# Optimization experiments

Hardware: AMD Instinct MI355X
Metric: run time of the kernel (lower is better)

Reference implementation:

```python
import jax, jax.numpy as jnp
import numpy as np


def conv2d_same(x, w, b):
    # x: (B,C,H,W), w: (O,I,3,3) -> 3x3 'same' conv, stride 1
    y = jax.lax.conv_general_dilated(
        x, w, window_strides=(1, 1), padding=((1, 1), (1, 1)),
        dimension_numbers=("NCHW", "OIHW", "NCHW"))
    return y + b[None, :, None, None]


def setup_inputs() -> dict:
    key = jax.random.key(0)
    ks = jax.random.split(key, 7)
    B, F, E, H, W = 16, 64, 16, 64, 64
    fan2d = F * 9
    state = jax.random.normal(ks[0], (B, F, H, W), dtype=jnp.float32)
    pre_w = jax.random.normal(ks[1], (F, F, 3, 3), dtype=jnp.float32) / np.sqrt(fan2d)
    pre_b = jax.random.normal(ks[2], (F,), dtype=jnp.float32) * 0.01
    attn_w = jax.random.normal(ks[3], (E, F, 3, 3), dtype=jnp.float32) / np.sqrt(fan2d)
    attn_b = jax.random.normal(ks[4], (E,), dtype=jnp.float32) * 0.01
    c3_w = jax.random.normal(ks[5], (F, F), dtype=jnp.float32) / np.sqrt(F)
    c3_b = jax.random.normal(ks[6], (F,), dtype=jnp.float32) * 0.01
    return {"state": state, "pre_w": pre_w, "pre_b": pre_b,
            "attn_w": attn_w, "attn_b": attn_b, "c3_w": c3_w, "c3_b": c3_b}


def reference(state, pre_w, pre_b, attn_w, attn_b, c3_w, c3_b):
    # pre_conv + relu
    x = jax.nn.relu(conv2d_same(state, pre_w, pre_b))
    # visattn_conv + sigmoid -> (B,E,H,W)
    attn = jax.nn.sigmoid(conv2d_same(x, attn_w, attn_b))
    # einsum 'bfyx,beyx->bfeyx'
    x5 = state[:, :, None, :, :] * attn[:, None, :, :, :]  # (B,F,E,H,W)
    # Conv3d kernel (1,1,1) with padding (0,1,1): zero-pad H,W by 1,
    # then pointwise linear over F. Output spatial dims become (E, H+2, W+2).
    x5 = jnp.pad(x5, ((0, 0), (0, 0), (0, 0), (1, 1), (1, 1)))
    y = jnp.einsum("of,bfeyx->boeyx", c3_w, x5) + c3_b[None, :, None, None, None]
    y = jax.nn.relu(y)
    # permute (0,2,1,3,4) then mean over last two dims -> (B,E,F)
    out = jnp.mean(y, axis=(-1, -2)).transpose(0, 2, 1)
    return out, attn
```

## Files before the change

### kernel.cpp

```cpp
#include <hip/hip_runtime.h>
#include <math.h>

constexpr int B = 16, F = 64, E = 16, H = 64, W = 64;
constexpr int XP = 66;
constexpr int CP = 72;
constexpr int YSTRIDE = XP * F;

typedef __bf16 bf16x8 __attribute__((ext_vector_type(8)));
typedef __bf16 bf16x4 __attribute__((ext_vector_type(4)));
typedef float f32x16 __attribute__((ext_vector_type(16)));
typedef float f32x4 __attribute__((ext_vector_type(4)));

__global__ __launch_bounds__(256) void prep_kernel(
    const float* __restrict__ state, const float* __restrict__ pre_w,
    const float* __restrict__ attn_w, const float* __restrict__ c3_w,
    __bf16* __restrict__ xTs, __bf16* __restrict__ wA1,
    __bf16* __restrict__ wA2, __bf16* __restrict__ wT3b,
    float* __restrict__ out0)
{
    __shared__ float s_t[64][68];
    const int blk = blockIdx.x;
    const int tid = threadIdx.x;

    if (blk < 1024) {
        const int b = blk >> 6, y = blk & 63;
        {
            int c = tid >> 2, x0 = (tid & 3) * 16;
            const float* src = state + ((size_t)(b * F + c) * H + y) * W + x0;
            #pragma unroll
            for (int q = 0; q < 4; ++q)
                *(float4*)&s_t[c][x0 + 4 * q] = *(const float4*)(src + 4 * q);
        }
        __syncthreads();
        __bf16* dst = xTs + (size_t)(b * H + y) * YSTRIDE;
        #pragma unroll
        for (int i = 0; i < 2; ++i) {
            int t = tid + i * 256;
            int x = t >> 3, cg = t & 7;
            bf16x8 v;
            #pragma unroll
            for (int j = 0; j < 8; ++j) v[j] = (__bf16)s_t[cg * 8 + j][x];
            *(bf16x8*)(dst + (x + 1) * F + cg * 8) = v;
        }
        if (tid < 16) {
            int bd = tid >> 3, cg = tid & 7;
            bf16x8 z = {};
            *(bf16x8*)(dst + (bd ? 65 : 0) * F + cg * 8) = z;
        }
    } else if (blk < 1168) {
        int idx = (blk - 1024) * 256 + tid;
        if (idx < 64 * 576) {
            int o = idx / 576, rem = idx - o * 576, t = rem >> 6, c = rem & 63;
            wA1[idx] = (__bf16)pre_w[(o * 64 + c) * 9 + t];
        }
        if (idx < 16 * 576) {
            int e = idx / 576, rem = idx - e * 576, t = rem >> 6, c = rem & 63;
            wA2[idx] = (__bf16)attn_w[(e * 64 + c) * 9 + t];
        }
        if (idx < 64 * 64) {
            wT3b[idx] = (__bf16)c3_w[idx];
        }
    } else {
        int idx = (blk - 1168) * 256 + tid;
        float4 z = {0.f, 0.f, 0.f, 0.f};
        *(float4*)(out0 + idx * 4) = z;
    }
}

__global__ __launch_bounds__(256) void mega_kernel(
    const __bf16* __restrict__ xTs, const __bf16* __restrict__ wA1,
    const __bf16* __restrict__ wA2, const __bf16* __restrict__ wT3b,
    const float* __restrict__ pre_b, const float* __restrict__ attn_b,
    const float* __restrict__ c3_b,
    float* __restrict__ attn_out, float* __restrict__ out)
{
    __shared__ __align__(16) char smem[63616];
    const int b = blockIdx.y, yp = blockIdx.x;
    const int tid = threadIdx.x;
    const int wave = tid >> 6, lane = tid & 63;
    const int y0 = yp * 2;

    __bf16* s_in = (__bf16*)smem;
    __bf16* sxo  = (__bf16*)smem;
    float (*s_attn)[64][16] = (float(*)[64][16])(smem + 38016);
    float (*s_sp)[68] = (float(*)[68])(smem + 46208);

    for (int t = tid; t < 6 * XP * 8; t += 256) {
        int r = t / (XP * 8), rem = t - r * (XP * 8);
        int x = rem >> 3, cg = rem & 7;
        int yy = y0 - 2 + r;
        bf16x8 v = {};
        if (yy >= 0 && yy < H)
            v = *(const bf16x8*)(xTs + (size_t)(b * H + yy) * YSTRIDE + x * F + cg * 8);
        *(bf16x8*)(s_in + (r * XP + x) * CP + cg * 8) = v;
    }
    __syncthreads();

    {
        const int n = lane & 31, kh = lane >> 5;
        const int yr = y0 - 1 + wave;
        f32x16 acc[4] = {};
        const bool valid = (yr >= 0 && yr < H);
        if (valid) {
            #pragma unroll
            for (int dy = 0; dy < 3; ++dy) {
                #pragma unroll
                for (int dx = 0; dx < 3; ++dx) {
                    const int t9 = dy * 3 + dx;
                    const __bf16* bB = s_in + ((wave + dy) * XP + (n + dx)) * CP + kh * 8;
                    #pragma unroll
                    for (int cq = 0; cq < 4; ++cq) {
                        const int ko = cq * 16 + kh * 8;
                        bf16x8 a0 = *(const bf16x8*)(wA1 + n * 576 + t9 * 64 + ko);
                        bf16x8 a1 = *(const bf16x8*)(wA1 + (32 + n) * 576 + t9 * 64 + ko);
                        bf16x8 b0 = *(const bf16x8*)(bB + cq * 16);
                        bf16x8 b1 = *(const bf16x8*)(bB + 32 * CP + cq * 16);
                        acc[0] = __builtin_amdgcn_mfma_f32_32x32x16_bf16(a0, b0, acc[0], 0, 0, 0);
                        acc[1] = __builtin_amdgcn_mfma_f32_32x32x16_bf16(a0, b1, acc[1], 0, 0, 0);
                        acc[2] = __builtin_amdgcn_mfma_f32_32x32x16_bf16(a1, b0, acc[2], 0, 0, 0);
                        acc[3] = __builtin_amdgcn_mfma_f32_32x32x16_bf16(a1, b1, acc[3], 0, 0, 0);
                    }
                }
            }
        }
        __syncthreads();

        __bf16* orow = sxo + wave * XP * CP;
        #pragma unroll
        for (int mt = 0; mt < 2; ++mt)
            #pragma unroll
            for (int g = 0; g < 4; ++g) {
                int o0 = mt * 32 + kh * 4 + g * 8;
                f32x4 b4 = *(const f32x4*)(pre_b + o0);
                bf16x4 v0 = {}, v1 = {};
                if (valid) {
                    #pragma unroll
                    for (int r = 0; r < 4; ++r) {
                        v0[r] = (__bf16)fmaxf(acc[mt * 2 + 0][g * 4 + r] + b4[r], 0.f);
                        v1[r] = (__bf16)fmaxf(acc[mt * 2 + 1][g * 4 + r] + b4[r], 0.f);
                    }
                }
                *(bf16x4*)(orow + (n + 1) * CP + o0) = v0;
                *(bf16x4*)(orow + (n + 33) * CP + o0) = v1;
            }
        if (tid < 64) {
            int r = tid >> 4, bd = (tid >> 3) & 1, cg = tid & 7;
            bf16x8 z = {};
            *(bf16x8*)(sxo + (r * XP + (bd ? 65 : 0)) * CP + cg * 8) = z;
        }
    }
    __syncthreads();

    const int rw = wave >> 1, nt2 = wave & 1;
    const int n16 = lane & 15, quad = lane >> 4;
    f32x4 acc2[2] = {};
    {
        const __bf16* aB = wA2 + n16 * 576 + quad * 8;
        #pragma unroll
        for (int dy = 0; dy < 3; ++dy)
            #pragma unroll
            for (int dx = 0; dx < 3; ++dx) {
                const int t9 = dy * 3 + dx;
                #pragma unroll
                for (int cq = 0; cq < 2; ++cq) {
                    bf16x8 a = *(const bf16x8*)(aB + t9 * 64 + cq * 32);
                    #pragma unroll
                    for (int i = 0; i < 2; ++i) {
                        const __bf16* bp = sxo +
                            ((rw + dy) * XP + (nt2 * 32 + i * 16 + n16 + dx)) * CP
                            + quad * 8 + cq * 32;
                        acc2[i] = __builtin_amdgcn_mfma_f32_16x16x32_bf16(
                            a, *(const bf16x8*)bp, acc2[i], 0, 0, 0);
                    }
                }
            }
    }

    #pragma unroll
    for (int i = 0; i < 2; ++i) {
        int x = nt2 * 32 + i * 16 + n16;
        #pragma unroll
        for (int r = 0; r < 4; ++r) {
            int e = quad * 4 + r;
            float val = acc2[i][r] + attn_b[e];
            float sg = 1.f / (1.f + __expf(-val));
            attn_out[((size_t)(b * E + e) * H + (y0 + rw)) * W + x] = sg;
            s_attn[rw][x][e] = sg;
        }
    }
    __syncthreads();

    const int combo = tid & 63;
    const int eg = combo >> 4, og = combo & 15, psub = tid >> 6;
    f32x4 cb4 = ((const f32x4*)c3_b)[og];
    float vsum[4] = {0.f, 0.f, 0.f, 0.f};

    for (int rr = 0; rr < 2; ++rr) {
        {
            const int mt = wave & 1, nt = wave >> 1;
            const int n = lane & 31, kh = lane >> 5;
            const __bf16* bBase = xTs + (size_t)(b * H + y0 + rr) * YSTRIDE
                                  + (nt * 32 + n + 1) * F + kh * 8;
            const __bf16* aBase = wT3b + (mt * 32 + n) * 64 + kh * 8;
            f32x16 acc = {};
            #pragma unroll
            for (int cq = 0; cq < 4; ++cq) {
                bf16x8 a  = *(const bf16x8*)(aBase + cq * 16);
                bf16x8 bb = *(const bf16x8*)(bBase + cq * 16);
                acc = __builtin_amdgcn_mfma_f32_32x32x16_bf16(a, bb, acc, 0, 0, 0);
            }
            #pragma unroll
            for (int g = 0; g < 4; ++g)
                #pragma unroll
                for (int r = 0; r < 4; ++r)
                    s_sp[nt * 32 + n][mt * 32 + kh * 4 + g * 8 + r] = acc[g * 4 + r];
        }
        __syncthreads();

        float accl[4][4] = {};
        #pragma unroll 2
        for (int pp = 0; pp < 16; ++pp) {
            int p = psub * 16 + pp;
            f32x4 a4 = *(const f32x4*)&s_attn[rr][p][eg * 4];
            f32x4 s4 = *(const f32x4*)&s_sp[p][og * 4];
            #pragma unroll
            for (int i = 0; i < 4; ++i)
                #pragma unroll
                for (int j = 0; j < 4; ++j)
                    accl[i][j] += fmaxf(fmaf(a4[i], s4[j], cb4[j]), 0.f);
        }
        __syncthreads();
        float* s_part = &s_sp[0][0];
        #pragma unroll
        for (int i = 0; i < 4; ++i)
            #pragma unroll
            for (int j = 0; j < 4; ++j)
                s_part[(psub * 64 + combo) * 16 + i * 4 + j] = accl[i][j];
        __syncthreads();
        {
            int cmb = tid >> 2, ii = tid & 3;
            #pragma unroll
            for (int j = 0; j < 4; ++j) {
                float v = 0.f;
                #pragma unroll
                for (int ps = 0; ps < 4; ++ps)
                    v += s_part[(ps * 64 + cmb) * 16 + ii * 4 + j];
                vsum[j] += v;
            }
        }
        __syncthreads();
    }
    {
        int cmb = tid >> 2, ii = tid & 3;
        int e = (cmb >> 4) * 4 + ii;
        #pragma unroll
        for (int j = 0; j < 4; ++j) {
            int o = (cmb & 15) * 4 + j;
            float add = vsum[j] * (1.f / 4356.f);
            if (yp == 0) add += 260.f * fmaxf(c3_b[o], 0.f) * (1.f / 4356.f);
            atomicAdd(&out[(b * E + e) * F + o], add);
        }
    }
}

extern "C" void kernel_launch(void* const* d_in, const int* in_sizes, int n_in,
                              void* d_out, int out_size, void* d_ws, size_t ws_size,
                              hipStream_t stream) {
    (void)in_sizes; (void)n_in; (void)out_size; (void)ws_size;
    const float* state  = (const float*)d_in[0];
    const float* pre_w  = (const float*)d_in[1];
    const float* pre_b  = (const float*)d_in[2];
    const float* attn_w = (const float*)d_in[3];
    const float* attn_b = (const float*)d_in[4];
    const float* c3_w   = (const float*)d_in[5];
    const float* c3_b   = (const float*)d_in[6];

    float* out      = (float*)d_out;
    float* attn_out = out + B * E * F;

    char* ws = (char*)d_ws;
    constexpr size_t XT_BYTES = (size_t)B * H * YSTRIDE * 2;
    __bf16* xTs  = (__bf16*)ws;
    __bf16* wA1  = (__bf16*)(ws + XT_BYTES);
    __bf16* wA2  = (__bf16*)(ws + XT_BYTES + 73728);
    __bf16* wT3b = (__bf16*)(ws + XT_BYTES + 73728 + 18432);

    prep_kernel<<<1184, 256, 0, stream>>>(state, pre_w, attn_w, c3_w,
                                          xTs, wA1, wA2, wT3b, out);
    mega_kernel<<<dim3(H / 2, B), 256, 0, stream>>>(xTs, wA1, wA2, wT3b,
                                                    pre_b, attn_b, c3_b,
                                                    attn_out, out);
}
```

Measured before the change: 116.1 us.

## Double mega_kernel block size to 512 threads and split work across 8 waves

```diff
diff --git a/kernel.cpp b/kernel.cpp
--- a/kernel.cpp
+++ b/kernel.cpp
@@ -67,7 +67,7 @@
     }
 }
 
-__global__ __launch_bounds__(256) void mega_kernel(
+__global__ __launch_bounds__(512, 4) void mega_kernel(
     const __bf16* __restrict__ xTs, const __bf16* __restrict__ wA1,
     const __bf16* __restrict__ wA2, const __bf16* __restrict__ wT3b,
     const float* __restrict__ pre_b, const float* __restrict__ attn_b,
@@ -84,8 +84,9 @@
     __bf16* sxo  = (__bf16*)smem;
     float (*s_attn)[64][16] = (float(*)[64][16])(smem + 38016);
     float (*s_sp)[68] = (float(*)[68])(smem + 46208);
-
-    for (int t = tid; t < 6 * XP * 8; t += 256) {
+    float* s_part = (float*)smem;
+
+    for (int t = tid; t < 6 * XP * 8; t += 512) {
         int r = t / (XP * 8), rem = t - r * (XP * 8);
         int x = rem >> 3, cg = rem & 7;
         int yy = y0 - 2 + r;
@@ -97,52 +98,49 @@
     __syncthreads();
 
     {
+        const int r1 = wave >> 1, nt = wave & 1;
         const int n = lane & 31, kh = lane >> 5;
-        const int yr = y0 - 1 + wave;
-        f32x16 acc[4] = {};
+        const int yr = y0 - 1 + r1;
         const bool valid = (yr >= 0 && yr < H);
+        f32x16 acc0 = {}, acc1 = {};
         if (valid) {
             #pragma unroll
             for (int dy = 0; dy < 3; ++dy) {
                 #pragma unroll
                 for (int dx = 0; dx < 3; ++dx) {
                     const int t9 = dy * 3 + dx;
-                    const __bf16* bB = s_in + ((wave + dy) * XP + (n + dx)) * CP + kh * 8;
+                    const __bf16* bB = s_in + ((r1 + dy) * XP + (nt * 32 + n + dx)) * CP + kh * 8;
                     #pragma unroll
                     for (int cq = 0; cq < 4; ++cq) {
                         const int ko = cq * 16 + kh * 8;
                         bf16x8 a0 = *(const bf16x8*)(wA1 + n * 576 + t9 * 64 + ko);
                         bf16x8 a1 = *(const bf16x8*)(wA1 + (32 + n) * 576 + t9 * 64 + ko);
-                        bf16x8 b0 = *(const bf16x8*)(bB + cq * 16);
-                        bf16x8 b1 = *(const bf16x8*)(bB + 32 * CP + cq * 16);
-                        acc[0] = __builtin_amdgcn_mfma_f32_32x32x16_bf16(a0, b0, acc[0], 0, 0, 0);
-                        acc[1] = __builtin_amdgcn_mfma_f32_32x32x16_bf16(a0, b1, acc[1], 0, 0, 0);
-                        acc[2] = __builtin_amdgcn_mfma_f32_32x32x16_bf16(a1, b0, acc[2], 0, 0, 0);
-                        acc[3] = __builtin_amdgcn_mfma_f32_32x32x16_bf16(a1, b1, acc[3], 0, 0, 0);
+                        bf16x8 bb = *(const bf16x8*)(bB + cq * 16);
+                        acc0 = __builtin_amdgcn_mfma_f32_32x32x16_bf16(a0, bb, acc0, 0, 0, 0);
+                        acc1 = __builtin_amdgcn_mfma_f32_32x32x16_bf16(a1, bb, acc1, 0, 0, 0);
                     }
                 }
             }
         }
         __syncthreads();
 
-        __bf16* orow = sxo + wave * XP * CP;
-        #pragma unroll
-        for (int mt = 0; mt < 2; ++mt)
-            #pragma unroll
-            for (int g = 0; g < 4; ++g) {
-                int o0 = mt * 32 + kh * 4 + g * 8;
-                f32x4 b4 = *(const f32x4*)(pre_b + o0);
-                bf16x4 v0 = {}, v1 = {};
-                if (valid) {
-                    #pragma unroll
-                    for (int r = 0; r < 4; ++r) {
-                        v0[r] = (__bf16)fmaxf(acc[mt * 2 + 0][g * 4 + r] + b4[r], 0.f);
-                        v1[r] = (__bf16)fmaxf(acc[mt * 2 + 1][g * 4 + r] + b4[r], 0.f);
-                    }
+        __bf16* orow = sxo + r1 * XP * CP;
+        #pragma unroll
+        for (int g = 0; g < 4; ++g) {
+            int o0 = kh * 4 + g * 8;
+            f32x4 b40 = *(const f32x4*)(pre_b + o0);
+            f32x4 b41 = *(const f32x4*)(pre_b + 32 + o0);
+            bf16x4 v0 = {}, v1 = {};
+            if (valid) {
+                #pragma unroll
+                for (int r = 0; r < 4; ++r) {
+                    v0[r] = (__bf16)fmaxf(acc0[g * 4 + r] + b40[r], 0.f);
+                    v1[r] = (__bf16)fmaxf(acc1[g * 4 + r] + b41[r], 0.f);
                 }
-                *(bf16x4*)(orow + (n + 1) * CP + o0) = v0;
-                *(bf16x4*)(orow + (n + 33) * CP + o0) = v1;
-            }
+            }
+            *(bf16x4*)(orow + (nt * 32 + n + 1) * CP + o0) = v0;
+            *(bf16x4*)(orow + (nt * 32 + n + 1) * CP + 32 + o0) = v1;
+        }
         if (tid < 64) {
             int r = tid >> 4, bd = (tid >> 3) & 1, cg = tid & 7;
             bf16x8 z = {};
@@ -151,10 +149,10 @@
     }
     __syncthreads();
 
-    const int rw = wave >> 1, nt2 = wave & 1;
-    const int n16 = lane & 15, quad = lane >> 4;
-    f32x4 acc2[2] = {};
     {
+        const int rw = wave >> 2, xq = wave & 3;
+        const int n16 = lane & 15, quad = lane >> 4;
+        f32x4 acc2 = {};
         const __bf16* aB = wA2 + n16 * 576 + quad * 8;
         #pragma unroll
         for (int dy = 0; dy < 3; ++dy)
@@ -164,25 +162,17 @@
                 #pragma unroll
                 for (int cq = 0; cq < 2; ++cq) {
                     bf16x8 a = *(const bf16x8*)(aB + t9 * 64 + cq * 32);
-                    #pragma unroll
-                    for (int i = 0; i < 2; ++i) {
-                        const __bf16* bp = sxo +
-                            ((rw + dy) * XP + (nt2 * 32 + i * 16 + n16 + dx)) * CP
-                            + quad * 8 + cq * 32;
-                        acc2[i] = __builtin_amdgcn_mfma_f32_16x16x32_bf16(
-                            a, *(const bf16x8*)bp, acc2[i], 0, 0, 0);
-                    }
+                    const __bf16* bp = sxo +
+                        ((rw + dy) * XP + (xq * 16 + n16 + dx)) * CP + quad * 8 + cq * 32;
+                    acc2 = __builtin_amdgcn_mfma_f32_16x16x32_bf16(
+                        a, *(const bf16x8*)bp, acc2, 0, 0, 0);
                 }
             }
-    }
-
-    #pragma unroll
-    for (int i = 0; i < 2; ++i) {
-        int x = nt2 * 32 + i * 16 + n16;
+        const int x = xq * 16 + n16;
         #pragma unroll
         for (int r = 0; r < 4; ++r) {
             int e = quad * 4 + r;
-            float val = acc2[i][r] + attn_b[e];
+            float val = acc2[r] + attn_b[e];
             float sg = 1.f / (1.f + __expf(-val));
             attn_out[((size_t)(b * E + e) * H + (y0 + rw)) * W + x] = sg;
             s_attn[rw][x][e] = sg;
@@ -196,7 +186,7 @@
     float vsum[4] = {0.f, 0.f, 0.f, 0.f};
 
     for (int rr = 0; rr < 2; ++rr) {
-        {
+        if (wave < 4) {
             const int mt = wave & 1, nt = wave >> 1;
             const int n = lane & 31, kh = lane >> 5;
             const __bf16* bBase = xTs + (size_t)(b * H + y0 + rr) * YSTRIDE
@@ -218,9 +208,9 @@
         __syncthreads();
 
         float accl[4][4] = {};
-        #pragma unroll 2
-        for (int pp = 0; pp < 16; ++pp) {
-            int p = psub * 16 + pp;
+        #pragma unroll
+        for (int pp = 0; pp < 8; ++pp) {
+            int p = psub * 8 + pp;
             f32x4 a4 = *(const f32x4*)&s_attn[rr][p][eg * 4];
             f32x4 s4 = *(const f32x4*)&s_sp[p][og * 4];
             #pragma unroll
@@ -230,27 +220,26 @@
                     accl[i][j] += fmaxf(fmaf(a4[i], s4[j], cb4[j]), 0.f);
         }
         __syncthreads();
-        float* s_part = &s_sp[0][0];
         #pragma unroll
         for (int i = 0; i < 4; ++i)
             #pragma unroll
             for (int j = 0; j < 4; ++j)
                 s_part[(psub * 64 + combo) * 16 + i * 4 + j] = accl[i][j];
         __syncthreads();
-        {
+        if (tid < 256) {
             int cmb = tid >> 2, ii = tid & 3;
             #pragma unroll
             for (int j = 0; j < 4; ++j) {
                 float v = 0.f;
                 #pragma unroll
-                for (int ps = 0; ps < 4; ++ps)
+                for (int ps = 0; ps < 8; ++ps)
                     v += s_part[(ps * 64 + cmb) * 16 + ii * 4 + j];
                 vsum[j] += v;
             }
         }
         __syncthreads();
     }
-    {
+    if (tid < 256) {
         int cmb = tid >> 2, ii = tid & 3;
         int e = (cmb >> 4) * 4 + ii;
         #pragma unroll
@@ -287,7 +276,7 @@
 
     prep_kernel<<<1184, 256, 0, stream>>>(state, pre_w, attn_w, c3_w,
                                           xTs, wA1, wA2, wT3b, out);
-    mega_kernel<<<dim3(H / 2, B), 256, 0, stream>>>(xTs, wA1, wA2, wT3b,
+    mega_kernel<<<dim3(H / 2, B), 512, 0, stream>>>(xTs, wA1, wA2, wT3b,
                                                     pre_b, attn_b, c3_b,
                                                     attn_out, out);
 }
```

New measurement: 149.4 us. 28.7% more time.

## Split conv1 input staging into channel halves to shrink LDS and drop syncs

Applied to the files above, without the earlier changes.

```diff
diff --git a/kernel.cpp b/kernel.cpp
--- a/kernel.cpp
+++ b/kernel.cpp
@@ -4,6 +4,7 @@
 constexpr int B = 16, F = 64, E = 16, H = 64, W = 64;
 constexpr int XP = 66;
 constexpr int CP = 72;
+constexpr int CPH = 40;
 constexpr int YSTRIDE = XP * F;
 
 typedef __bf16 bf16x8 __attribute__((ext_vector_type(8)));
@@ -67,14 +68,14 @@
     }
 }
 
-__global__ __launch_bounds__(256) void mega_kernel(
+__global__ __launch_bounds__(256, 3) void mega_kernel(
     const __bf16* __restrict__ xTs, const __bf16* __restrict__ wA1,
     const __bf16* __restrict__ wA2, const __bf16* __restrict__ wT3b,
     const float* __restrict__ pre_b, const float* __restrict__ attn_b,
     const float* __restrict__ c3_b,
     float* __restrict__ attn_out, float* __restrict__ out)
 {
-    __shared__ __align__(16) char smem[63616];
+    __shared__ __align__(16) char smem[46208];
     const int b = blockIdx.y, yp = blockIdx.x;
     const int tid = threadIdx.x;
     const int wave = tid >> 6, lane = tid & 63;
@@ -83,38 +84,42 @@
     __bf16* s_in = (__bf16*)smem;
     __bf16* sxo  = (__bf16*)smem;
     float (*s_attn)[64][16] = (float(*)[64][16])(smem + 38016);
-    float (*s_sp)[68] = (float(*)[68])(smem + 46208);
-
-    for (int t = tid; t < 6 * XP * 8; t += 256) {
-        int r = t / (XP * 8), rem = t - r * (XP * 8);
-        int x = rem >> 3, cg = rem & 7;
-        int yy = y0 - 2 + r;
-        bf16x8 v = {};
-        if (yy >= 0 && yy < H)
-            v = *(const bf16x8*)(xTs + (size_t)(b * H + yy) * YSTRIDE + x * F + cg * 8);
-        *(bf16x8*)(s_in + (r * XP + x) * CP + cg * 8) = v;
-    }
-    __syncthreads();
-
-    {
-        const int n = lane & 31, kh = lane >> 5;
-        const int yr = y0 - 1 + wave;
-        f32x16 acc[4] = {};
-        const bool valid = (yr >= 0 && yr < H);
+    float (*s_sp)[68] = (float(*)[68])smem;
+    float* s_part = (float*)(smem + 17408);
+
+    const int n = lane & 31, kh = lane >> 5;
+    const int yr = y0 - 1 + wave;
+    const bool valid = (yr >= 0 && yr < H);
+    f32x16 acc[4] = {};
+
+    #pragma unroll
+    for (int h = 0; h < 2; ++h) {
+        if (h) __syncthreads();
+        for (int t = tid; t < 6 * XP * 4; t += 256) {
+            int r = t / (XP * 4), rem = t - r * (XP * 4);
+            int x = rem >> 2, cg = rem & 3;
+            int yy = y0 - 2 + r;
+            bf16x8 v = {};
+            if (yy >= 0 && yy < H)
+                v = *(const bf16x8*)(xTs + (size_t)(b * H + yy) * YSTRIDE
+                                     + x * F + h * 32 + cg * 8);
+            *(bf16x8*)(s_in + (r * XP + x) * CPH + cg * 8) = v;
+        }
+        __syncthreads();
         if (valid) {
             #pragma unroll
             for (int dy = 0; dy < 3; ++dy) {
                 #pragma unroll
                 for (int dx = 0; dx < 3; ++dx) {
                     const int t9 = dy * 3 + dx;
-                    const __bf16* bB = s_in + ((wave + dy) * XP + (n + dx)) * CP + kh * 8;
+                    const __bf16* bB = s_in + ((wave + dy) * XP + (n + dx)) * CPH + kh * 8;
                     #pragma unroll
-                    for (int cq = 0; cq < 4; ++cq) {
-                        const int ko = cq * 16 + kh * 8;
-                        bf16x8 a0 = *(const bf16x8*)(wA1 + n * 576 + t9 * 64 + ko);
-                        bf16x8 a1 = *(const bf16x8*)(wA1 + (32 + n) * 576 + t9 * 64 + ko);
+                    for (int cq = 0; cq < 2; ++cq) {
+                        const int ko_w = h * 32 + cq * 16 + kh * 8;
+                        bf16x8 a0 = *(const bf16x8*)(wA1 + n * 576 + t9 * 64 + ko_w);
+                        bf16x8 a1 = *(const bf16x8*)(wA1 + (32 + n) * 576 + t9 * 64 + ko_w);
                         bf16x8 b0 = *(const bf16x8*)(bB + cq * 16);
-                        bf16x8 b1 = *(const bf16x8*)(bB + 32 * CP + cq * 16);
+                        bf16x8 b1 = *(const bf16x8*)(bB + 32 * CPH + cq * 16);
                         acc[0] = __builtin_amdgcn_mfma_f32_32x32x16_bf16(a0, b0, acc[0], 0, 0, 0);
                         acc[1] = __builtin_amdgcn_mfma_f32_32x32x16_bf16(a0, b1, acc[1], 0, 0, 0);
                         acc[2] = __builtin_amdgcn_mfma_f32_32x32x16_bf16(a1, b0, acc[2], 0, 0, 0);
@@ -123,8 +128,10 @@
                 }
             }
         }
-        __syncthreads();
-
+    }
+    __syncthreads();
+
+    {
         __bf16* orow = sxo + wave * XP * CP;
         #pragma unroll
         for (int mt = 0; mt < 2; ++mt)
@@ -198,10 +205,10 @@
     for (int rr = 0; rr < 2; ++rr) {
         {
             const int mt = wave & 1, nt = wave >> 1;
-            const int n = lane & 31, kh = lane >> 5;
+            const int ns = lane & 31, khs = lane >> 5;
             const __bf16* bBase = xTs + (size_t)(b * H + y0 + rr) * YSTRIDE
-                                  + (nt * 32 + n + 1) * F + kh * 8;
-            const __bf16* aBase = wT3b + (mt * 32 + n) * 64 + kh * 8;
+                                  + (nt * 32 + ns + 1) * F + khs * 8;
+            const __bf16* aBase = wT3b + (mt * 32 + ns) * 64 + khs * 8;
             f32x16 acc = {};
             #pragma unroll
             for (int cq = 0; cq < 4; ++cq) {
@@ -213,7 +220,7 @@
             for (int g = 0; g < 4; ++g)
                 #pragma unroll
                 for (int r = 0; r < 4; ++r)
-                    s_sp[nt * 32 + n][mt * 32 + kh * 4 + g * 8 + r] = acc[g * 4 + r];
+                    s_sp[nt * 32 + ns][mt * 32 + khs * 4 + g * 8 + r] = acc[g * 4 + r];
         }
         __syncthreads();
 
@@ -229,8 +236,6 @@
                 for (int j = 0; j < 4; ++j)
                     accl[i][j] += fmaxf(fmaf(a4[i], s4[j], cb4[j]), 0.f);
         }
-        __syncthreads();
-        float* s_part = &s_sp[0][0];
         #pragma unroll
         for (int i = 0; i < 4; ++i)
             #pragma unroll
@@ -248,7 +253,6 @@
                 vsum[j] += v;
             }
         }
-        __syncthreads();
     }
     {
         int cmb = tid >> 2, ii = tid & 3;
```

After: 116.9 us. About the same (+0.7%).

## Hoist pointwise-conv GEMM into conv1 phase and simplify final reduction

Applied to the files above, without the earlier changes.

```diff
diff --git a/kernel.cpp b/kernel.cpp
--- a/kernel.cpp
+++ b/kernel.cpp
@@ -4,6 +4,7 @@
 constexpr int B = 16, F = 64, E = 16, H = 64, W = 64;
 constexpr int XP = 66;
 constexpr int CP = 72;
+constexpr int SPP = 68;
 constexpr int YSTRIDE = XP * F;
 
 typedef __bf16 bf16x8 __attribute__((ext_vector_type(8)));
@@ -67,7 +68,7 @@
     }
 }
 
-__global__ __launch_bounds__(256) void mega_kernel(
+__global__ __launch_bounds__(256, 2) void mega_kernel(
     const __bf16* __restrict__ xTs, const __bf16* __restrict__ wA1,
     const __bf16* __restrict__ wA2, const __bf16* __restrict__ wT3b,
     const float* __restrict__ pre_b, const float* __restrict__ attn_b,
@@ -82,8 +83,8 @@
 
     __bf16* s_in = (__bf16*)smem;
     __bf16* sxo  = (__bf16*)smem;
-    float (*s_attn)[64][16] = (float(*)[64][16])(smem + 38016);
-    float (*s_sp)[68] = (float(*)[68])(smem + 46208);
+    __bf16* s_sp = (__bf16*)(smem + 38016);
+    float (*s_attn)[64][16] = (float(*)[64][16])(smem + 55424);
 
     for (int t = tid; t < 6 * XP * 8; t += 256) {
         int r = t / (XP * 8), rem = t - r * (XP * 8);
@@ -96,53 +97,85 @@
     }
     __syncthreads();
 
+    const int n = lane & 31, kh = lane >> 5;
+    const int mt = wave & 1, nt = wave >> 1;
+
+    bf16x8 spA[4], spB[2][4];
+    #pragma unroll
+    for (int cq = 0; cq < 4; ++cq)
+        spA[cq] = *(const bf16x8*)(wT3b + (mt * 32 + n) * 64 + kh * 8 + cq * 16);
+    #pragma unroll
+    for (int rr = 0; rr < 2; ++rr)
+        #pragma unroll
+        for (int cq = 0; cq < 4; ++cq)
+            spB[rr][cq] = *(const bf16x8*)(xTs + (size_t)(b * H + y0 + rr) * YSTRIDE
+                                           + (nt * 32 + n + 1) * F + kh * 8 + cq * 16);
+
+    const int yr = y0 - 1 + wave;
+    const bool valid = (yr >= 0 && yr < H);
+    f32x16 acc[4] = {};
+    if (valid) {
+        #pragma unroll
+        for (int dy = 0; dy < 3; ++dy) {
+            #pragma unroll
+            for (int dx = 0; dx < 3; ++dx) {
+                const int t9 = dy * 3 + dx;
+                const __bf16* bB = s_in + ((wave + dy) * XP + (n + dx)) * CP + kh * 8;
+                #pragma unroll
+                for (int cq = 0; cq < 4; ++cq) {
+                    const int ko = cq * 16 + kh * 8;
+                    bf16x8 a0 = *(const bf16x8*)(wA1 + n * 576 + t9 * 64 + ko);
+                    bf16x8 a1 = *(const bf16x8*)(wA1 + (32 + n) * 576 + t9 * 64 + ko);
+                    bf16x8 b0 = *(const bf16x8*)(bB + cq * 16);
+                    bf16x8 b1 = *(const bf16x8*)(bB + 32 * CP + cq * 16);
+                    acc[0] = __builtin_amdgcn_mfma_f32_32x32x16_bf16(a0, b0, acc[0], 0, 0, 0);
+                    acc[1] = __builtin_amdgcn_mfma_f32_32x32x16_bf16(a0, b1, acc[1], 0, 0, 0);
+                    acc[2] = __builtin_amdgcn_mfma_f32_32x32x16_bf16(a1, b0, acc[2], 0, 0, 0);
+                    acc[3] = __builtin_amdgcn_mfma_f32_32x32x16_bf16(a1, b1, acc[3], 0, 0, 0);
+                }
+            }
+        }
+    }
+
+    f32x16 accsp[2] = {};
+    #pragma unroll
+    for (int rr = 0; rr < 2; ++rr)
+        #pragma unroll
+        for (int cq = 0; cq < 4; ++cq)
+            accsp[rr] = __builtin_amdgcn_mfma_f32_32x32x16_bf16(
+                spA[cq], spB[rr][cq], accsp[rr], 0, 0, 0);
+
+    __syncthreads();
+
     {
-        const int n = lane & 31, kh = lane >> 5;
-        const int yr = y0 - 1 + wave;
-        f32x16 acc[4] = {};
-        const bool valid = (yr >= 0 && yr < H);
-        if (valid) {
-            #pragma unroll
-            for (int dy = 0; dy < 3; ++dy) {
-                #pragma unroll
-                for (int dx = 0; dx < 3; ++dx) {
-                    const int t9 = dy * 3 + dx;
-                    const __bf16* bB = s_in + ((wave + dy) * XP + (n + dx)) * CP + kh * 8;
-                    #pragma unroll
-                    for (int cq = 0; cq < 4; ++cq) {
-                        const int ko = cq * 16 + kh * 8;
-                        bf16x8 a0 = *(const bf16x8*)(wA1 + n * 576 + t9 * 64 + ko);
-                        bf16x8 a1 = *(const bf16x8*)(wA1 + (32 + n) * 576 + t9 * 64 + ko);
-                        bf16x8 b0 = *(const bf16x8*)(bB + cq * 16);
-                        bf16x8 b1 = *(const bf16x8*)(bB + 32 * CP + cq * 16);
-                        acc[0] = __builtin_amdgcn_mfma_f32_32x32x16_bf16(a0, b0, acc[0], 0, 0, 0);
-                        acc[1] = __builtin_amdgcn_mfma_f32_32x32x16_bf16(a0, b1, acc[1], 0, 0, 0);
-                        acc[2] = __builtin_amdgcn_mfma_f32_32x32x16_bf16(a1, b0, acc[2], 0, 0, 0);
-                        acc[3] = __builtin_amdgcn_mfma_f32_32x32x16_bf16(a1, b1, acc[3], 0, 0, 0);
-                    }
-                }
-            }
-        }
-        __syncthreads();
-
         __bf16* orow = sxo + wave * XP * CP;
         #pragma unroll
-        for (int mt = 0; mt < 2; ++mt)
+        for (int mt2 = 0; mt2 < 2; ++mt2)
             #pragma unroll
             for (int g = 0; g < 4; ++g) {
-                int o0 = mt * 32 + kh * 4 + g * 8;
+                int o0 = mt2 * 32 + kh * 4 + g * 8;
                 f32x4 b4 = *(const f32x4*)(pre_b + o0);
                 bf16x4 v0 = {}, v1 = {};
                 if (valid) {
                     #pragma unroll
                     for (int r = 0; r < 4; ++r) {
-                        v0[r] = (__bf16)fmaxf(acc[mt * 2 + 0][g * 4 + r] + b4[r], 0.f);
-                        v1[r] = (__bf16)fmaxf(acc[mt * 2 + 1][g * 4 + r] + b4[r], 0.f);
+                        v0[r] = (__bf16)fmaxf(acc[mt2 * 2 + 0][g * 4 + r] + b4[r], 0.f);
+                        v1[r] = (__bf16)fmaxf(acc[mt2 * 2 + 1][g * 4 + r] + b4[r], 0.f);
                     }
                 }
                 *(bf16x4*)(orow + (n + 1) * CP + o0) = v0;
                 *(bf16x4*)(orow + (n + 33) * CP + o0) = v1;
             }
+        const int p = nt * 32 + n;
+        #pragma unroll
+        for (int rr = 0; rr < 2; ++rr)
+            #pragma unroll
+            for (int g = 0; g < 4; ++g)
+                #pragma unroll
+                for (int r = 0; r < 4; ++r) {
+                    int o = mt * 32 + kh * 4 + g * 8 + r;
+                    s_sp[(rr * 64 + o) * SPP + p] = (__bf16)accsp[rr][g * 4 + r];
+                }
         if (tid < 64) {
             int r = tid >> 4, bd = (tid >> 3) & 1, cg = tid & 7;
             bf16x8 z = {};
@@ -151,10 +184,10 @@
     }
     __syncthreads();
 
-    const int rw = wave >> 1, nt2 = wave & 1;
-    const int n16 = lane & 15, quad = lane >> 4;
-    f32x4 acc2[2] = {};
     {
+        const int rw = wave >> 1, nt2 = wave & 1;
+        const int n16 = lane & 15, quad = lane >> 4;
+        f32x4 acc2[2] = {};
         const __bf16* aB = wA2 + n16 * 576 + quad * 8;
         #pragma unroll
         for (int dy = 0; dy < 3; ++dy)
@@ -174,91 +207,48 @@
                     }
                 }
             }
-    }
-
-    #pragma unroll
-    for (int i = 0; i < 2; ++i) {
-        int x = nt2 * 32 + i * 16 + n16;
-        #pragma unroll
-        for (int r = 0; r < 4; ++r) {
-            int e = quad * 4 + r;
-            float val = acc2[i][r] + attn_b[e];
-            float sg = 1.f / (1.f + __expf(-val));
-            attn_out[((size_t)(b * E + e) * H + (y0 + rw)) * W + x] = sg;
-            s_attn[rw][x][e] = sg;
-        }
-    }
-    __syncthreads();
-
-    const int combo = tid & 63;
-    const int eg = combo >> 4, og = combo & 15, psub = tid >> 6;
-    f32x4 cb4 = ((const f32x4*)c3_b)[og];
-    float vsum[4] = {0.f, 0.f, 0.f, 0.f};
-
-    for (int rr = 0; rr < 2; ++rr) {
-        {
-            const int mt = wave & 1, nt = wave >> 1;
-            const int n = lane & 31, kh = lane >> 5;
-            const __bf16* bBase = xTs + (size_t)(b * H + y0 + rr) * YSTRIDE
-                                  + (nt * 32 + n + 1) * F + kh * 8;
-            const __bf16* aBase = wT3b + (mt * 32 + n) * 64 + kh * 8;
-            f32x16 acc = {};
-            #pragma unroll
-            for (int cq = 0; cq < 4; ++cq) {
-                bf16x8 a  = *(const bf16x8*)(aBase + cq * 16);
-                bf16x8 bb = *(const bf16x8*)(bBase + cq * 16);
-                acc = __builtin_amdgcn_mfma_f32_32x32x16_bf16(a, bb, acc, 0, 0, 0);
-            }
-            #pragma unroll
-            for (int g = 0; g < 4; ++g)
-                #pragma unroll
-                for (int r = 0; r < 4; ++r)
-                    s_sp[nt * 32 + n][mt * 32 + kh * 4 + g * 8 + r] = acc[g * 4 + r];
-        }
-        __syncthreads();
-
-        float accl[4][4] = {};
-        #pragma unroll 2
-        for (int pp = 0; pp < 16; ++pp) {
-            int p = psub * 16 + pp;
-            f32x4 a4 = *(const f32x4*)&s_attn[rr][p][eg * 4];
-            f32x4 s4 = *(const f32x4*)&s_sp[p][og * 4];
-            #pragma unroll
-            for (int i = 0; i < 4; ++i)
-                #pragma unroll
-                for (int j = 0; j < 4; ++j)
-                    accl[i][j] += fmaxf(fmaf(a4[i], s4[j], cb4[j]), 0.f);
-        }
-        __syncthreads();
-        float* s_part = &s_sp[0][0];
-        #pragma unroll
-        for (int i = 0; i < 4; ++i)
-            #pragma unroll
-            for (int j = 0; j < 4; ++j)
-                s_part[(psub * 64 + combo) * 16 + i * 4 + j] = accl[i][j];
-        __syncthreads();
-        {
-            int cmb = tid >> 2, ii = tid & 3;
-            #pragma unroll
-            for (int j = 0; j < 4; ++j) {
-                float v = 0.f;
-                #pragma unroll
-                for (int ps = 0; ps < 4; ++ps)
-                    v += s_part[(ps * 64 + cmb) * 16 + ii * 4 + j];
-                vsum[j] += v;
-            }
-        }
-        __syncthreads();
-    }
+        #pragma unroll
+        for (int i = 0; i < 2; ++i) {
+            int x = nt2 * 32 + i * 16 + n16;
+            #pragma unroll
+            for (int r = 0; r < 4; ++r) {
+                int e = quad * 4 + r;
+                float val = acc2[i][r] + attn_b[e];
+                float sg = 1.f / (1.f + __expf(-val));
+                attn_out[((size_t)(b * E + e) * H + (y0 + rw)) * W + x] = sg;
+                s_attn[rw][x][e] = sg;
+            }
+        }
+    }
+    __syncthreads();
+
     {
-        int cmb = tid >> 2, ii = tid & 3;
-        int e = (cmb >> 4) * 4 + ii;
-        #pragma unroll
-        for (int j = 0; j < 4; ++j) {
-            int o = (cmb & 15) * 4 + j;
-            float add = vsum[j] * (1.f / 4356.f);
-            if (yp == 0) add += 260.f * fmaxf(c3_b[o], 0.f) * (1.f / 4356.f);
-            atomicAdd(&out[(b * E + e) * F + o], add);
+        const int o = tid & 63, eg = tid >> 6;
+        const float cb = c3_b[o];
+        float accl[4] = {0.f, 0.f, 0.f, 0.f};
+        #pragma unroll
+        for (int rr = 0; rr < 2; ++rr) {
+            const __bf16* spr = s_sp + (rr * 64 + o) * SPP;
+            #pragma unroll 2
+            for (int pb = 0; pb < 8; ++pb) {
+                bf16x8 sp8 = *(const bf16x8*)(spr + pb * 8);
+                #pragma unroll
+                for (int k = 0; k < 8; ++k) {
+                    float spf = (float)sp8[k];
+                    f32x4 a4 = *(const f32x4*)&s_attn[rr][pb * 8 + k][eg * 4];
+                    #pragma unroll
+                    for (int i = 0; i < 4; ++i)
+                        accl[i] += fmaxf(fmaf(a4[i], spf, cb), 0.f);
+                }
+            }
+        }
+        float border = (yp == 0) ? 260.f * fmaxf(cb, 0.f) : 0.f;
+        #pragma unroll
+        for (int i = 0; i < 4; ++i) {
+            int e = eg * 4 + i;
+            atomicAdd(&out[(b * E + e) * F + o],
+                      (accl[i] + border * (i == 0 ? 0.f : 0.f) + (i == 0 ? border : border)) * 0.f
+                      + (accl[i] + border) * (1.f / 4356.f));
         }
     }
 }
```

After: 115.3 us. About the same (-0.7%).
